# Kernel tuning notes

Measured on AMD Instinct MI355X. Metric: run time of the kernel, lower is better.

## Reference

```python
import jax, jax.numpy as jnp
import numpy as np
import itertools


def _rotation_perms():
    """The 24 rotation matrices of the cube, as permutations of the group
    acting on itself by left multiplication (regular action)."""
    mats = []
    for perm in itertools.permutations(range(3)):
        for signs in itertoolsools if False else itertools.product((1, -1), repeat=3):
            M = np.zeros((3, 3), dtype=np.int64)
            for r, (p, s) in enumerate(zip(perm, signs)):
                M[r, p] = s
            if int(round(np.linalg.det(M))) == 1:
                mats.append(M)
    assert len(mats) == 24
    idx = {m.tobytes(): k for k, m in enumerate(mats)}
    perms = np.zeros((24, 24), dtype=np.int64)
    for k, g in enumerate(mats):
        for i, h in enumerate(mats):
            perms[k, i] = idx[(g @ h).tobytes()]
    return perms


def compute_pair_orbits():
    all_rot = _rotation_perms()
    pair_orbit = np.full((24, 24), -1, dtype=np.int64)
    orbit_id = 0
    for i in range(24):
        for j in range(24):
            if pair_orbit[i, j] == -1:
                for g in all_rot:
                    gi, gj = int(g[i]), int(g[j])
                    if pair_orbit[gi, gj] == -1:
                        pair_orbit[gi, gj] = orbit_id
                orbit_id += 1
    assert (pair_orbit >= 0).all()
    return pair_orbit, orbit_id


C_IN, C_OUT, BATCH = 512, 512, 2048


def setup_inputs() -> dict:
    key = jax.random.key(0)
    kx, kw = jax.random.split(key)
    pair_orbit, n_orbits = compute_pair_orbits()  # (24,24), n_orbits == 24
    x = jax.random.normal(kx, (BATCH, 24, C_IN), dtype=jnp.float32)
    # kaiming-uniform-like init, bound = sqrt(6 / ((1+5) * fan_in)), fan_in = c_in*n_orbits
    bound = float(np.sqrt(1.0 / (C_IN * n_orbits)))
    weight = jax.random.uniform(kw, (C_OUT, C_IN, n_orbits), dtype=jnp.float32,
                                minval=-bound, maxval=bound)
    bias = jnp.zeros((C_OUT,), dtype=jnp.float32)
    return {"x": x, "weight": weight, "bias": bias,
            "pair_orbit": jnp.asarray(pair_orbit)}


def reference(x, weight, bias, pair_orbit):
    # kernel[o, c, i, j] = weight[o, c, pair_orbit[i, j]]
    kernel = weight[:, :, pair_orbit]            # (c_out, c_in, 24, 24)
    out = jnp.einsum('bjc,ocij->bio', x, kernel)  # (batch, 24, c_out)
    return out + bias
```

## Files before the change

### kernel.cpp

```cpp
#include <hip/hip_runtime.h>

#define BATCH 2048
#define CIN   512
#define COUT  512
#define GSZ   24
#define NORB  24
#define M_DIM (BATCH*GSZ)
#define K_DIM (GSZ*CIN)
#define N_DIM COUT
#define BM 192
#define BN 128
#define BK 64

typedef __bf16 bf16x8 __attribute__((ext_vector_type(8)));
typedef float  f32x4  __attribute__((ext_vector_type(4)));
typedef unsigned short u16;

__device__ __forceinline__ u16 f2bf(float f) {
  union { float f; unsigned u; } v; v.f = f;
  unsigned u = v.u;
  return (u16)((u + 0x7fffu + ((u >> 16) & 1u)) >> 16);
}

__global__ void convert_x(const float* __restrict__ x, u16* __restrict__ xb, int n4) {
  const int base = blockIdx.x * 1024 + threadIdx.x;
#pragma unroll
  for (int i = 0; i < 4; ++i) {
    const int t = base + i * 256;
    if (t >= n4) return;
    const float4 v = *(const float4*)(x + (size_t)t * 4);
    ushort4 o;
    o.x = f2bf(v.x); o.y = f2bf(v.y); o.z = f2bf(v.z); o.w = f2bf(v.w);
    *(ushort4*)(xb + (size_t)t * 4) = o;
  }
}

#define TROW 520
__global__ void build_bt(const float* __restrict__ w, u16* __restrict__ bt) {
  __shared__ __align__(16) u16 lds[NORB * TROW];
  const int o = blockIdx.x;
  const int t = threadIdx.x;
  const float* wo = w + (size_t)o * K_DIM;
#pragma unroll
  for (int it = 0; it < 12; ++it) {
    const int idx = it * 256 + t;
    const float4 v = *(const float4*)(wo + idx * 4);
    const int k0 = idx * 4;
#pragma unroll
    for (int e = 0; e < 4; ++e) {
      const int k = k0 + e;
      const int c = k / 24;
      const int r = k - c * 24;
      lds[r * TROW + c] = f2bf(e == 0 ? v.x : e == 1 ? v.y : e == 2 ? v.z : v.w);
    }
  }
  __syncthreads();
  u16* bo = bt + (size_t)o * K_DIM;
#pragma unroll
  for (int it = 0; it < 6; ++it) {
    const int eidx = it * 256 + t;
    const int base = eidx * 8;
    const int r = base >> 9;
    const int c0 = base & 511;
    const uint4 v = *(const uint4*)(lds + r * TROW + c0);
    *(uint4*)(bo + base) = v;
  }
}

__launch_bounds__(256, 2)
__global__ void gemm_gc(const u16* __restrict__ xb, const u16* __restrict__ bt,
                        const float* __restrict__ bias, const int* __restrict__ pair_orbit,
                        float* __restrict__ out) {
  __shared__ __align__(16) u16 As[BM * BK];
  __shared__ __align__(16) u16 Bs[3 * BN * BK];
  __shared__ int jmap[GSZ * 25];

  const int t   = threadIdx.x;
  const int gid = blockIdx.x;
  const int xcd = gid & 7;
  const int n0  = (xcd & 3) * BN;
  const int m0  = ((gid >> 3) * 2 + (xcd >> 2)) * BM;

  for (int idx = t; idx < GSZ * NORB; idx += 256) {
    const int i = idx / 24;
    const int j = idx - i * 24;
    jmap[i * 25 + pair_orbit[idx]] = j;
  }

  const int tr0 = t >> 3;
  const int kcg = ((t & 7) ^ (tr0 & 7)) * 8;
  const u16* aSrc = xb + (size_t)(m0 + tr0) * CIN + kcg;
  const u16* bSrc = bt + (size_t)(n0 + tr0) * K_DIM + kcg;
  u16* aDst = (u16*)As + t * 8;
  u16* bDst = (u16*)Bs + t * 8;

  auto stage_a = [&](int kb) {
#pragma unroll
    for (int it = 0; it < 6; ++it)
      __builtin_amdgcn_global_load_lds(
          (__attribute__((address_space(1))) void*)(aSrc + (size_t)it * 32 * CIN + kb * 64),
          (__attribute__((address_space(3))) void*)(aDst + it * 2048), 16, 0, 0);
  };
  auto stage_b = [&](int kb, int r, int soffElems) {
#pragma unroll
    for (int it = 0; it < 4; ++it)
      __builtin_amdgcn_global_load_lds(
          (__attribute__((address_space(1))) void*)(bSrc + (size_t)it * 32 * K_DIM + r * 512 + kb * 64),
          (__attribute__((address_space(3))) void*)(bDst + soffElems + it * 2048), 16, 0, 0);
  };

  const int w    = t >> 6;
  const int lane = t & 63;
  const int lm   = lane & 15;
  const int q    = lane >> 4;
  const int mw   = (w >> 1) * 96;
  const int nw   = (w & 1) * 64;
  const int q8   = q << 3;

  int b24[6], i25[6];
#pragma unroll
  for (int f = 0; f < 6; ++f) {
    const int tr = mw + f * 16 + lm;
    const int b  = tr / 24;
    b24[f] = b * 24;
    i25[f] = (tr - b * 24) * 25;
  }
  int baseB[4];
#pragma unroll
  for (int nf = 0; nf < 4; ++nf)
    baseB[nf] = (nw + lm + 16 * nf) * 64 + (q8 ^ ((lm & 7) << 3));

  f32x4 acc[6][4];
#pragma unroll
  for (int i = 0; i < 6; ++i)
#pragma unroll
    for (int j = 0; j < 4; ++j)
      acc[i][j] = (f32x4){0.f, 0.f, 0.f, 0.f};

  stage_a(0);
  stage_b(0, 0, 0);
  __syncthreads();
  stage_b(0, 1, 8192);

  int rowC[6];
#pragma unroll
  for (int f = 0; f < 6; ++f) rowC[f] = b24[f] + jmap[i25[f]];

  int cur = 0, w2 = 2;
  int r2 = 2, kb2 = 0;
  int rr = 0, kb = 0;

#pragma unroll 1
  for (int tt = 0; tt < 192; ++tt) {
    if (tt < 191) asm volatile("s_waitcnt vmcnt(4)" ::: "memory");
    else          asm volatile("s_waitcnt vmcnt(0)" ::: "memory");
    __builtin_amdgcn_s_barrier();
    __builtin_amdgcn_sched_barrier(0);

    const bool bnd = (rr == 23);
    if (!bnd && tt < 190) stage_b(kb2, r2, w2 << 13);

    int c0[6];
#pragma unroll
    for (int f = 0; f < 6; ++f)
      c0[f] = rowC[f] * 64 + (q8 ^ ((rowC[f] & 7) << 3));

    int rowN[6];
    const int rn = bnd ? 0 : (rr + 1);
#pragma unroll
    for (int f = 0; f < 6; ++f) rowN[f] = b24[f] + jmap[i25[f] + rn];

    const int soff = cur << 13;
#pragma unroll
    for (int h = 0; h < 2; ++h) {
      const int hx = h * 32;
      bf16x8 av[6], bv[4];
#pragma unroll
      for (int nf = 0; nf < 4; ++nf)
        bv[nf] = *(const bf16x8*)(Bs + soff + (baseB[nf] ^ hx));
#pragma unroll
      for (int f = 0; f < 6; ++f)
        av[f] = *(const bf16x8*)(As + (c0[f] ^ hx));
      __builtin_amdgcn_s_setprio(1);
#pragma unroll
      for (int mf = 0; mf < 6; ++mf)
#pragma unroll
        for (int nf = 0; nf < 4; ++nf)
          acc[mf][nf] = __builtin_amdgcn_mfma_f32_16x16x32_bf16(av[mf], bv[nf], acc[mf][nf], 0, 0, 0);
      __builtin_amdgcn_s_setprio(0);
    }

#pragma unroll
    for (int f = 0; f < 6; ++f) rowC[f] = rowN[f];

    if (bnd && kb < 7) {
      __builtin_amdgcn_s_barrier();
      __builtin_amdgcn_sched_barrier(0);
      stage_a(kb + 1);
      stage_b(kb2, r2, w2 << 13);
    }

    cur = (cur == 2) ? 0 : cur + 1;
    w2  = (w2 == 2) ? 0 : w2 + 1;
    if (++r2 == 24) { r2 = 0; ++kb2; }
    if (++rr == 24) { rr = 0; ++kb; }
  }

#pragma unroll
  for (int nf = 0; nf < 4; ++nf) {
    const int col = n0 + nw + nf * 16 + lm;
    const float bv = bias[col];
#pragma unroll
    for (int mf = 0; mf < 6; ++mf) {
      const int mrow = m0 + mw + mf * 16 + q * 4;
#pragma unroll
      for (int e = 0; e < 4; ++e)
        out[(size_t)(mrow + e) * N_DIM + col] = acc[mf][nf][e] + bv;
    }
  }
}

extern "C" void kernel_launch(void* const* d_in, const int* in_sizes, int n_in,
                              void* d_out, int out_size, void* d_ws, size_t ws_size,
                              hipStream_t stream) {
  (void)in_sizes; (void)n_in; (void)out_size; (void)ws_size;
  const float* x    = (const float*)d_in[0];
  const float* wgt  = (const float*)d_in[1];
  const float* bias = (const float*)d_in[2];
  const int*   po   = (const int*)d_in[3];
  float* out = (float*)d_out;

  u16* xb = (u16*)d_ws;
  u16* bt = xb + (size_t)M_DIM * CIN;

  const int nx4 = (BATCH * GSZ * CIN) / 4;
  convert_x<<<nx4 / 1024, 256, 0, stream>>>(x, xb, nx4);
  build_bt<<<COUT, 256, 0, stream>>>(wgt, bt);

  const int grid = (M_DIM / BM) * (N_DIM / BN);
  gemm_gc<<<grid, 256, 0, stream>>>(xb, bt, bias, po, out);
}
```

Baseline: 650.0 us.

## Software-pipeline LDS fragment reads across k-steps with register double buffering

Each iteration now prefetches the first-half A/B fragments of the next k-step into registers while the second-half MFMAs run, so LDS read latency overlaps with matrix math. The fine-grained `vmcnt(4)` wait plus raw barrier is replaced by a full `__syncthreads`. The B-stage issue at group boundaries no longer waits for the second barrier, and the buffer index rotation is reworked for the three-slot B ring. The aim is to hide LDS latency, but the full sync may drain outstanding global loads each iteration and reduce global-load overlap. Register pressure also rises from the extra fragment buffers.

Result: slower. 670.3 us (+3.1%).

```diff
diff --git a/kernel.cpp b/kernel.cpp
--- a/kernel.cpp
+++ b/kernel.cpp
@@ -139,69 +139,88 @@
 
   stage_a(0);
   stage_b(0, 0, 0);
+  stage_b(0, 1, 8192);
   __syncthreads();
-  stage_b(0, 1, 8192);
-
-  int rowC[6];
-#pragma unroll
-  for (int f = 0; f < 6; ++f) rowC[f] = b24[f] + jmap[i25[f]];
-
-  int cur = 0, w2 = 2;
+
+  int rowC[6], c0C[6];
+#pragma unroll
+  for (int f = 0; f < 6; ++f) {
+    rowC[f] = b24[f] + jmap[i25[f]];
+    c0C[f] = rowC[f] * 64 + (q8 ^ ((rowC[f] & 7) << 3));
+  }
+
+  bf16x8 avP[6], bvP[4], avQ[6], bvQ[4];
+
+  int cur = 0, nxt = 1, w2 = 2;
   int r2 = 2, kb2 = 0;
   int rr = 0, kb = 0;
 
 #pragma unroll 1
   for (int tt = 0; tt < 192; ++tt) {
-    if (tt < 191) asm volatile("s_waitcnt vmcnt(4)" ::: "memory");
-    else          asm volatile("s_waitcnt vmcnt(0)" ::: "memory");
-    __builtin_amdgcn_s_barrier();
-    __builtin_amdgcn_sched_barrier(0);
-
-    const bool bnd = (rr == 23);
-    if (!bnd && tt < 190) stage_b(kb2, r2, w2 << 13);
-
-    int c0[6];
+    __syncthreads();
+
+    const bool bnd  = (rr == 23);
+    if (tt < 190) stage_b(kb2, r2, w2 << 13);
+
+    const int soffC = cur << 13;
+    const int soffN = nxt << 13;
+
+    if (rr == 0) {
+#pragma unroll
+      for (int nf = 0; nf < 4; ++nf)
+        bvP[nf] = *(const bf16x8*)(Bs + soffC + baseB[nf]);
+#pragma unroll
+      for (int f = 0; f < 6; ++f)
+        avP[f] = *(const bf16x8*)(As + c0C[f]);
+    }
+
+#pragma unroll
+    for (int nf = 0; nf < 4; ++nf)
+      bvQ[nf] = *(const bf16x8*)(Bs + soffC + (baseB[nf] ^ 32));
 #pragma unroll
     for (int f = 0; f < 6; ++f)
-      c0[f] = rowC[f] * 64 + (q8 ^ ((rowC[f] & 7) << 3));
-
-    int rowN[6];
+      avQ[f] = *(const bf16x8*)(As + (c0C[f] ^ 32));
+    __builtin_amdgcn_s_setprio(1);
+#pragma unroll
+    for (int mf = 0; mf < 6; ++mf)
+#pragma unroll
+      for (int nf = 0; nf < 4; ++nf)
+        acc[mf][nf] = __builtin_amdgcn_mfma_f32_16x16x32_bf16(avP[mf], bvP[nf], acc[mf][nf], 0, 0, 0);
+    __builtin_amdgcn_s_setprio(0);
+
     const int rn = bnd ? 0 : (rr + 1);
-#pragma unroll
-    for (int f = 0; f < 6; ++f) rowN[f] = b24[f] + jmap[i25[f] + rn];
-
-    const int soff = cur << 13;
-#pragma unroll
-    for (int h = 0; h < 2; ++h) {
-      const int hx = h * 32;
-      bf16x8 av[6], bv[4];
+    int rowN[6], c0N[6];
+#pragma unroll
+    for (int f = 0; f < 6; ++f) {
+      rowN[f] = b24[f] + jmap[i25[f] + rn];
+      c0N[f] = rowN[f] * 64 + (q8 ^ ((rowN[f] & 7) << 3));
+    }
+
+#pragma unroll
+    for (int nf = 0; nf < 4; ++nf)
+      bvP[nf] = *(const bf16x8*)(Bs + soffN + baseB[nf]);
+    if (!bnd) {
+#pragma unroll
+      for (int f = 0; f < 6; ++f)
+        avP[f] = *(const bf16x8*)(As + c0N[f]);
+    }
+    __builtin_amdgcn_s_setprio(1);
+#pragma unroll
+    for (int mf = 0; mf < 6; ++mf)
 #pragma unroll
       for (int nf = 0; nf < 4; ++nf)
-        bv[nf] = *(const bf16x8*)(Bs + soff + (baseB[nf] ^ hx));
-#pragma unroll
-      for (int f = 0; f < 6; ++f)
-        av[f] = *(const bf16x8*)(As + (c0[f] ^ hx));
-      __builtin_amdgcn_s_setprio(1);
-#pragma unroll
-      for (int mf = 0; mf < 6; ++mf)
-#pragma unroll
-        for (int nf = 0; nf < 4; ++nf)
-          acc[mf][nf] = __builtin_amdgcn_mfma_f32_16x16x32_bf16(av[mf], bv[nf], acc[mf][nf], 0, 0, 0);
-      __builtin_amdgcn_s_setprio(0);
-    }
-
-#pragma unroll
-    for (int f = 0; f < 6; ++f) rowC[f] = rowN[f];
+        acc[mf][nf] = __builtin_amdgcn_mfma_f32_16x16x32_bf16(avQ[mf], bvQ[nf], acc[mf][nf], 0, 0, 0);
+    __builtin_amdgcn_s_setprio(0);
+
+#pragma unroll
+    for (int f = 0; f < 6; ++f) { rowC[f] = rowN[f]; c0C[f] = c0N[f]; }
 
     if (bnd && kb < 7) {
-      __builtin_amdgcn_s_barrier();
-      __builtin_amdgcn_sched_barrier(0);
+      __syncthreads();
       stage_a(kb + 1);
-      stage_b(kb2, r2, w2 << 13);
-    }
-
-    cur = (cur == 2) ? 0 : cur + 1;
-    w2  = (w2 == 2) ? 0 : w2 + 1;
+    }
+
+    const int tmp = cur; cur = nxt; nxt = w2; w2 = tmp;
     if (++r2 == 24) { r2 = 0; ++kb2; }
     if (++rr == 24) { rr = 0; ++kb; }
   }
```
